# Kernel optimization log

Hardware: AMD Instinct MI355X
Metric: run time of the kernel (lower is better)

The kernel has to match this reference:

```python
import jax, jax.numpy as jnp
import numpy as np

N, C_IN, C_OUT, T, V = 128, 64, 64, 128, 25
GROUPS, K = 8, 3
REL = C_IN // 8  # rel_reduction=8, in_channels>16


def setup_inputs() -> dict:
    key = jax.random.key(0)
    ks = jax.random.split(key, 16)
    f = lambda k, sh, s=0.05: (jax.random.normal(k, sh) * s).astype(jnp.float32)
    return {
        "x0": jax.random.normal(ks[0], (N, C_IN, T, V), jnp.float32),
        "DecoupleA": f(ks[1], (K, GROUPS, V, V), 0.2),
        "A": f(ks[2], (K, V, V), 0.2),
        "alpha": jnp.full((1,), 0.5, jnp.float32),
        "w1": f(ks[3], (K, REL, C_IN)), "b1": f(ks[4], (K, REL)),
        "w2": f(ks[5], (K, REL, C_IN)), "b2": f(ks[6], (K, REL)),
        "w3": f(ks[7], (K, C_OUT, C_IN)), "b3": f(ks[8], (K, C_OUT)),
        "w4": f(ks[9], (K, C_OUT, REL)), "b4": f(ks[10], (K, C_OUT)),
        "Linear_weight": f(ks[11], (C_IN, C_OUT * K)),
        "Linear_bias": f(ks[12], (1, C_OUT * K, 1, 1)),
        "bn0_gamma": jnp.ones((C_OUT * K,), jnp.float32),
        "bn0_beta": jnp.zeros((C_OUT * K,), jnp.float32),
        "ens_w": f(ks[13], (C_OUT, 2 * C_OUT)), "ens_b": f(ks[14], (C_OUT,)),
        "bn_gamma": jnp.full((C_OUT,), 1e-6, jnp.float32),
        "bn_beta": jnp.zeros((C_OUT,), jnp.float32),
    }


def _bn(x, gamma, beta, eps=1e-5):
    # training-mode BatchNorm2d over NCHW: stats over (N, T, V)
    mu = x.mean(axis=(0, 2, 3), keepdims=True)
    var = x.var(axis=(0, 2, 3), keepdims=True)
    return (x - mu) * jax.lax.rsqrt(var + eps) * gamma[None, :, None, None] + beta[None, :, None, None]


def _norm_adj(A):
    # torch: D = A.sum(dim=rows) -> column sums; A @ diag(1/(D+1e-3)) scales columns
    d = A.sum(axis=-2)  # [..., V] column sums
    return A * (1.0 / (d + 0.001))[..., None, :]


def reference(x0, DecoupleA, A, alpha, w1, b1, w2, b2, w3, b3, w4, b4,
              Linear_weight, Linear_bias, bn0_gamma, bn0_beta, ens_w, ens_b,
              bn_gamma, bn_beta):
    n, c_in, t, v = x0.shape
    k, g = DecoupleA.shape[0], DecoupleA.shape[1]
    c_out = w3.shape[1]
    # DecoupleA.repeat(1, out_channels//groups, 1, 1) == tile along channel dim
    learn_A = jnp.tile(DecoupleA, (1, c_out // g, 1, 1))  # [K, C_OUT, V, V]
    norm_A = _norm_adj(learn_A)
    # decoupled linear path
    x = jnp.einsum('nctv,cd->ndtv', x0, Linear_weight) + Linear_bias
    x = _bn(x, bn0_gamma, bn0_beta)
    x = x.reshape(n, k, c_out, t, v)
    x = jnp.einsum('nkctv,kcvw->nctw', x, norm_A)  # [n, C_OUT, t, v]
    # CTRGC branches (conv-then-mean over T == mean-then-1x1 since conv is linear)
    xm = x0.mean(axis=2)  # [n, c_in, v]
    y = jnp.zeros((n, c_out, t, v), x0.dtype)
    for i in range(k):
        x1 = jnp.einsum('ncv,rc->nrv', xm, w1[i]) + b1[i][:, None]
        x2 = jnp.einsum('ncv,rc->nrv', xm, w2[i]) + b2[i][:, None]
        diff = jnp.tanh(x1[:, :, :, None] - x2[:, :, None, :])        # [n, rel, u, w]
        att = jnp.einsum('nruw,or->nouw', diff, w4[i]) + b4[i][None, :, None, None]
        att = att * alpha[0] + A[i][None, None]                        # [n, C_OUT, u, w]
        x3 = jnp.einsum('nctv,oc->notv', x0, w3[i]) + b3[i][None, :, None, None]
        y = y + jnp.einsum('ncuv,nctu->nctv', att, x3)
    cat = jnp.concatenate([x, y], axis=1)                              # [n, 2*C_OUT, t, v]
    out = jnp.einsum('nctv,oc->notv', cat, ens_w) + ens_b[None, :, None, None]
    out = _bn(out, bn_gamma, bn_beta)
    out = out + x0  # down is identity since in_channels == out_channels
    return jax.nn.relu(out)
```

## Files before the change

kernel.cpp:

```cpp
#include <hip/hip_runtime.h>
#include <cstddef>
#include <cstring>

typedef _Float16 h8 __attribute__((ext_vector_type(8)));
typedef _Float16 h4v __attribute__((ext_vector_type(4)));
typedef float f4 __attribute__((ext_vector_type(4)));
typedef unsigned int u32;
typedef unsigned short u16;

#define MTOT 409600.0f

#define DO_XM  15360000
#define DO_GP  15564800
#define DO_GR  16613376

#define WS_OB16 0
#define WS_ATT  13631488
#define WS_ATTB 23461888
#define WS_BN2P 23666688
#define WS_PAR  23827456
#define WS_CSN  23828000

#define ATT_H 27262976
#define NAB_H 47595520
#define CB_H  47620096
#define WA_H  47622144
#define W3_H  47634432
#define EW_H  47646720

#define LDS_DYN 116736

__global__ __launch_bounds__(512) void k_gram(const float* __restrict__ x0,
                                              float* __restrict__ gp) {
  __shared__ _Float16 Xs[64 * 128];
  char* smb = (char*)Xs;
  int bid = blockIdx.x, tid = threadIdx.x;
  int n = bid >> 1, sh = bid & 1;
  int base = sh * 1536;
  int niter = sh ? 13 : 12;
  const float* xb = x0 + (size_t)n * 204800;
  int wid = tid >> 6, lane = tid & 63, l15 = lane & 15, l4 = lane >> 4;
  int ca = (wid & 3) * 16;
  int jb0 = (wid >> 2) * 2;
  f4 acc[2] = {{0.f, 0.f, 0.f, 0.f}, {0.f, 0.f, 0.f, 0.f}};
  int sc = tid >> 3, scol = (tid & 7) * 16;
  int swz = (sc & 7) << 4;
  for (int it = 0; it < niter; ++it) {
    int s0 = base + it * 128;
    __syncthreads();
    const float* src = xb + sc * 3200 + s0 + scol;
#pragma unroll
    for (int j = 0; j < 4; ++j) {
      float4 f = *(const float4*)(src + j * 4);
      h4v hv = {(_Float16)f.x, (_Float16)f.y, (_Float16)f.z, (_Float16)f.w};
      *(h4v*)(smb + sc * 256 + (((scol + j * 4) * 2) ^ swz)) = hv;
    }
    __syncthreads();
#pragma unroll
    for (int kk = 0; kk < 4; ++kk) {
      int kb = kk * 64 + l4 * 16;
      int arow = ca + l15;
      h8 af = *(const h8*)(smb + arow * 256 + (kb ^ ((arow & 7) << 4)));
#pragma unroll
      for (int j = 0; j < 2; ++j) {
        int brow = (jb0 + j) * 16 + l15;
        h8 bf = *(const h8*)(smb + brow * 256 + (kb ^ ((brow & 7) << 4)));
        acc[j] = __builtin_amdgcn_mfma_f32_16x16x32_f16(af, bf, acc[j], 0, 0, 0);
      }
    }
  }
  float* o = gp + (size_t)bid * 4096;
#pragma unroll
  for (int j = 0; j < 2; ++j)
#pragma unroll
    for (int q = 0; q < 4; ++q)
      o[(ca + l4 * 4 + q) * 64 + (jb0 + j) * 16 + l15] = acc[j][q];
}

__global__ __launch_bounds__(256) void k_gred(float* __restrict__ dsc) {
  int bid = blockIdx.x, tid = threadIdx.x;
  if (bid < 16) {
    int idx = bid * 256 + tid;
    const float* gp = dsc + DO_GP;
    float s0 = 0.f, s1 = 0.f, s2 = 0.f, s3 = 0.f;
    for (int b = 0; b < 256; b += 4) {
      s0 += gp[(size_t)b * 4096 + idx];
      s1 += gp[(size_t)(b + 1) * 4096 + idx];
      s2 += gp[(size_t)(b + 2) * 4096 + idx];
      s3 += gp[(size_t)(b + 3) * 4096 + idx];
    }
    dsc[DO_GR + idx] = (s0 + s1) + (s2 + s3);
  } else {
    __shared__ float red[64][5];
    int c = tid >> 2, j = tid & 3;
    float s = 0.f;
    for (int nn = j; nn < 128; nn += 4) {
      const float* xmp = dsc + DO_XM + (size_t)(nn * 64 + c) * 25;
      for (int v = 0; v < 25; ++v) s += xmp[v];
    }
    red[c][j] = s;
    __syncthreads();
    if (j == 0)
      dsc[DO_GR + 4096 + c] = 128.f * (red[c][0] + red[c][1] + red[c][2] + red[c][3]);
  }
}

__global__ __launch_bounds__(256) void k_xm(const float* __restrict__ x0,
                                            float* __restrict__ dsc,
                                            float* __restrict__ ws) {
  __shared__ float red[8][32];
  int bid = blockIdx.x;
  int gid = bid * 256 + threadIdx.x;
  if (gid < 204800) ws[WS_ATTB + gid] = 0.f;
  int n = bid >> 6, c = bid & 63;
  int tid = threadIdx.x;
  int tq = tid >> 5, v = tid & 31;
  const float* xb = x0 + (size_t)(n * 64 + c) * 3200;
  float s = 0.f;
  if (v < 25) {
    for (int j = 0; j < 16; j++) s += xb[(tq + 8 * j) * 25 + v];
  }
  red[tq][v] = s;
  __syncthreads();
  if (tq == 0 && v < 25) {
    float tot = 0.f;
#pragma unroll
    for (int q = 0; q < 8; q++) tot += red[q][v];
    dsc[DO_XM + (size_t)(n * 64 + c) * 25 + v] = tot * (1.0f / 128.0f);
  }
}

__global__ __launch_bounds__(256) void k_prep(const float* __restrict__ DA,
                                              const float* __restrict__ w3,
                                              const float* __restrict__ ensw,
                                              float* __restrict__ wsF) {
  int bid = blockIdx.x, tid = threadIdx.x;
  _Float16* wsH = (_Float16*)wsF;
  if (bid < 3) {
    if (tid < 200) {
      int k = bid, g = tid / 25, w = tid % 25;
      const float* base = DA + (k * 8 + g) * 625 + w;
      float s = 0.f;
      for (int v = 0; v < 25; v++) s += base[v * 25];
      float inv = 1.0f / (s + 0.001f);
      wsF[WS_CSN + k * 200 + g * 25 + w] = s * inv;
      _Float16* dst = wsH + NAB_H + (size_t)((k * 8 + g) * 32 + w) * 32;
      for (int v = 0; v < 25; v++) dst[v] = (_Float16)(base[v * 25] * inv);
      for (int v = 25; v < 32; v++) dst[v] = (_Float16)0.f;
    }
  } else if (bid == 3) {
    for (int idx = tid; idx < 5376; idx += 256) {
      int kg = idx / 224, r = idx % 224;
      int w = 25 + r / 32, v = r & 31;
      wsH[NAB_H + (size_t)(kg * 32 + w) * 32 + v] = (_Float16)0.f;
    }
  } else if (bid < 12) {
    int i0 = (bid - 4) * 1536;
    for (int i = tid; i < 1536; i += 256)
      wsH[W3_H + i0 + i] = (_Float16)w3[i0 + i];
  } else {
    int i0 = (bid - 12) * 2048;
    for (int i = tid; i < 2048; i += 256)
      wsH[EW_H + i0 + i] = (_Float16)ensw[i0 + i];
  }
}

__global__ __launch_bounds__(256) void k_bnstat(const float* __restrict__ dsc,
                                                const float* __restrict__ Lw,
                                                const float* __restrict__ g0,
                                                const float* __restrict__ b0,
                                                float* __restrict__ wsF) {
  __shared__ float Gsh[64 * 66];
  __shared__ float Ly[64][17];
  __shared__ float part[16][17];
  __shared__ float a1L[16];
  int bid = blockIdx.x, tid = threadIdx.x;
  int d0 = bid * 16, dl = tid >> 4, r = tid & 15, d = d0 + dl;
  for (int idx = tid; idx < 4096; idx += 256)
    Gsh[(idx >> 6) * 66 + (idx & 63)] = dsc[DO_GR + idx];
  for (int idx = tid; idx < 1024; idx += 256)
    Ly[idx >> 4][idx & 15] = Lw[(idx >> 4) * 192 + d0 + (idx & 15)];
  __syncthreads();
  float acc = 0.f;
#pragma unroll
  for (int cc = 0; cc < 4; ++cc) {
    int c = r * 4 + cc;
    float h = 0.f;
    for (int c2 = 0; c2 < 64; ++c2) h += Gsh[c * 66 + c2] * Ly[c2][dl];
    acc += Ly[c][dl] * h;
  }
  part[dl][r] = acc;
  __syncthreads();
  if (r == 0) {
    float ex2 = 0.f;
#pragma unroll
    for (int i = 0; i < 16; ++i) ex2 += part[dl][i];
    ex2 *= (1.0f / MTOT);
    float mu = 0.f;
    for (int c = 0; c < 64; ++c) mu += dsc[DO_GR + 4096 + c] * Ly[c][dl];
    mu *= (1.0f / MTOT);
    float var = ex2 - mu * mu;
    float a1 = g0[d] * rsqrtf(var + 1e-5f);
    float b1c = b0[d] - a1 * mu;
    wsF[WS_PAR + 128 + d] = a1;
    wsF[WS_PAR + 320 + d] = b1c;
    a1L[dl] = a1;
  }
  __syncthreads();
  _Float16* wsH = (_Float16*)wsF;
  int k = d >> 6, cg = d & 63;
  float a1v = a1L[dl];
#pragma unroll
  for (int j = 0; j < 4; ++j) {
    int e = r * 4 + j;
    wsH[WA_H + k * 4096 + cg * 64 + e] = (_Float16)(a1v * Lw[e * 192 + d]);
  }
}

__global__ __launch_bounds__(256) void k_cb(float* __restrict__ wsF) {
  int tid = threadIdx.x;
  _Float16* wsH = (_Float16*)wsF;
  for (int idx = tid; idx < 2048; idx += 256) {
    int c = idx >> 5, w = idx & 31;
    float s = 0.f;
    if (w < 25) {
      int g = c & 7;
      for (int k = 0; k < 3; ++k)
        s += wsF[WS_PAR + 320 + k * 64 + c] * wsF[WS_CSN + k * 200 + g * 25 + w];
    }
    wsH[CB_H + idx] = (_Float16)s;
  }
}

__global__ __launch_bounds__(256) void k_att(const float* __restrict__ dsc,
    const float* __restrict__ w1, const float* __restrict__ b1,
    const float* __restrict__ w2, const float* __restrict__ b2,
    const float* __restrict__ w4, const float* __restrict__ b4,
    const float* __restrict__ Ag, const float* __restrict__ alpha,
    const float* __restrict__ b3, float* __restrict__ wsF) {
  __shared__ float xms[1600];
  __shared__ float x1s[200];
  __shared__ float x2s[200];
  __shared__ float Td[5000];
  int bid = blockIdx.x, tid = threadIdx.x;
  int n = bid / 3, i = bid % 3;
  for (int idx = tid; idx < 1600; idx += 256)
    xms[idx] = dsc[DO_XM + (size_t)n * 1600 + idx];
  __syncthreads();
  for (int idx = tid; idx < 400; idx += 256) {
    int r = (idx % 200) / 25, u = idx % 25;
    const float* wv = (idx < 200 ? w1 : w2) + (i * 8 + r) * 64;
    float acc = (idx < 200 ? b1 : b2)[i * 8 + r];
    for (int c = 0; c < 64; c++) acc += xms[c * 25 + u] * wv[c];
    if (idx < 200) x1s[r * 25 + u] = acc; else x2s[r * 25 + u] = acc;
  }
  __syncthreads();
  for (int idx = tid; idx < 5000; idx += 256) {
    int r = idx / 625, u = (idx % 625) / 25, w = idx % 25;
    Td[idx] = tanhf(x1s[r * 25 + u] - x2s[r * 25 + w]);
  }
  __syncthreads();
  float al = alpha[0];
  u32* attW = (u32*)wsF;
  for (int p = tid; p < 1600; p += 256) {
    int o = p / 25, w = p % 25;
    float w4r[8];
#pragma unroll
    for (int r = 0; r < 8; r++) w4r[r] = w4[(i * 64 + o) * 8 + r];
    float b4v = b4[i * 64 + o];
    const float* AgW = Ag + i * 625 + w;
    float asum = 0.f;
    size_t rowH = (size_t)ATT_H + ((size_t)((n * 3 + i) * 64 + o) * 25 + w) * 32;
    u32* row = attW + rowH / 2;
    for (int up = 0; up < 16; ++up) {
      u32 word = 0;
#pragma unroll
      for (int h = 0; h < 2; ++h) {
        int u = up * 2 + h;
        float v = 0.f;
        if (u < 25) {
          float acc = b4v;
#pragma unroll
          for (int r = 0; r < 8; r++) acc += w4r[r] * Td[r * 625 + u * 25 + w];
          v = al * acc + AgW[u * 25];
          asum += v;
        }
        union { _Float16 hf; u16 b; } cv;
        cv.hf = (_Float16)v;
        word |= ((u32)cv.b) << (16 * h);
      }
      row[up] = word;
    }
    atomicAdd(&wsF[WS_ATTB + (size_t)n * 1600 + p], b3[i * 64 + o] * asum);
  }
}

__device__ __forceinline__ void stageX(const float* __restrict__ xn, char* sm, int tid) {
  for (int idx = tid; idx < 25600; idx += 512) {
    int c = idx / 400, s = idx % 400;
    float f = xn[c * 3200 + s];
    *(_Float16*)(sm + s * 128 + ((c * 2) ^ ((s & 7) << 4))) = (_Float16)f;
  }
}
__device__ __forceinline__ void zeroHpads(char* sm, int tid) {
  for (int idx = tid; idx < 7168; idx += 512) {
    int c = idx / 112, r = idx % 112;
    int t = r / 7, u = 25 + r % 7;
    int hs = (((t & 3) ^ ((c >> 2) & 3)) << 4);
    *(_Float16*)(sm + 51200 + c * 1024 + t * 64 + ((u * 2) ^ hs)) = (_Float16)0.f;
  }
}
__device__ __forceinline__ void gemm64(const _Float16* __restrict__ Aw, char* sm,
                                       int wid, int lane) {
  int l15 = lane & 15, l4 = lane >> 4;
  int mt = wid & 3, half = wid >> 2;
  h8 a0 = *(const h8*)(Aw + (mt * 16 + l15) * 64 + l4 * 8);
  h8 a1 = *(const h8*)(Aw + (mt * 16 + l15) * 64 + 32 + l4 * 8);
  int nt0 = half * 13, nt1 = 13 + half * 12;
  for (int nt = nt0; nt < nt1; ++nt) {
    int s = nt * 16 + l15;
    int sw = (s & 7) << 4;
    const char* rb = sm + s * 128;
    h8 b0 = *(const h8*)(rb + ((l4 * 16) ^ sw));
    h8 b1 = *(const h8*)(rb + ((64 + l4 * 16) ^ sw));
    f4 acc = {0.f, 0.f, 0.f, 0.f};
    acc = __builtin_amdgcn_mfma_f32_16x16x32_f16(a0, b0, acc, 0, 0, 0);
    acc = __builtin_amdgcn_mfma_f32_16x16x32_f16(a1, b1, acc, 0, 0, 0);
    int t = s / 25, u = s % 25;
#pragma unroll
    for (int q = 0; q < 4; ++q) {
      int c = mt * 16 + l4 * 4 + q;
      int hs = (((t & 3) ^ ((c >> 2) & 3)) << 4);
      *(_Float16*)(sm + 51200 + c * 1024 + t * 64 + ((u * 2) ^ hs)) = (_Float16)acc[q];
    }
  }
}

__global__ __launch_bounds__(512) void kAB(const float* __restrict__ x0,
                                           float* ws,
                                           const float* __restrict__ ensb) {
  extern __shared__ char sm[];
  __shared__ float redS[128];
  __shared__ float attBs[1600];
  const _Float16* wsH = (const _Float16*)ws;
  int tid = threadIdx.x, bid = blockIdx.x;
  int lb = (bid & 7) * 128 + (bid >> 3);
  int n = lb >> 3, tile = lb & 7;
  int wid = tid >> 6, lane = tid & 63, l15 = lane & 15, l4 = lane >> 4;
  if (tid < 128) redS[tid] = 0.f;
  for (int idx = tid; idx < 1600; idx += 512)
    attBs[idx] = ws[WS_ATTB + (size_t)n * 1600 + idx];
  stageX(x0 + (size_t)n * 204800 + tile * 400, sm, tid);
  zeroHpads(sm, tid);
  __syncthreads();
  f4 accx[8][2], accy[8][2];
#pragma unroll
  for (int a = 0; a < 8; a++)
#pragma unroll
    for (int b = 0; b < 2; b++) {
      accx[a][b] = (f4){0.f, 0.f, 0.f, 0.f};
      accy[a][b] = (f4){0.f, 0.f, 0.f, 0.f};
    }
  for (int k = 0; k < 3; ++k) {
    gemm64(wsH + WA_H + k * 4096, sm, wid, lane);
    __syncthreads();
#pragma unroll
    for (int mt2 = 0; mt2 < 8; ++mt2) {
      int c = mt2 * 8 + wid;
      int hs = (((l15 & 3) ^ ((c >> 2) & 3)) << 4);
      h8 aH = *(const h8*)(sm + 51200 + c * 1024 + l15 * 64 + ((l4 * 16) ^ hs));
#pragma unroll
      for (int nt2 = 0; nt2 < 2; ++nt2) {
        const _Float16* nb = wsH + NAB_H +
            (size_t)((k * 8 + wid) * 32 + nt2 * 16 + l15) * 32 + l4 * 8;
        accx[mt2][nt2] = __builtin_amdgcn_mfma_f32_16x16x32_f16(
            aH, *(const h8*)nb, accx[mt2][nt2], 0, 0, 0);
      }
    }
    __syncthreads();
  }
  for (int i = 0; i < 3; ++i) {
    gemm64(wsH + W3_H + i * 4096, sm, wid, lane);
    __syncthreads();
#pragma unroll
    for (int mt2 = 0; mt2 < 8; ++mt2) {
      int c = mt2 * 8 + wid;
      int hs = (((l15 & 3) ^ ((c >> 2) & 3)) << 4);
      h8 aX = *(const h8*)(sm + 51200 + c * 1024 + l15 * 64 + ((l4 * 16) ^ hs));
#pragma unroll
      for (int nt2 = 0; nt2 < 2; ++nt2) {
        int v = nt2 * 16 + l15;
        int vc = v < 25 ? v : 0;
        const _Float16* ab = wsH + ATT_H +
            ((size_t)((n * 3 + i) * 64 + c) * 25 + vc) * 32 + l4 * 8;
        accy[mt2][nt2] = __builtin_amdgcn_mfma_f32_16x16x32_f16(
            aX, *(const h8*)ab, accy[mt2][nt2], 0, 0, 0);
      }
    }
    __syncthreads();
  }
#pragma unroll
  for (int mt2 = 0; mt2 < 8; ++mt2) {
    int c = mt2 * 8 + wid;
#pragma unroll
    for (int nt2 = 0; nt2 < 2; ++nt2) {
      int w = nt2 * 16 + l15;
      if (w < 25) {
        float cbv = (float)wsH[CB_H + c * 32 + w];
        float abv = attBs[c * 25 + w];
#pragma unroll
        for (int q = 0; q < 4; ++q) {
          int t = l4 * 4 + q;
          int s = t * 25 + w;
          int sw = (s & 7) << 4;
          *(_Float16*)(sm + s * 256 + ((c * 2) ^ sw)) =
              (_Float16)(accx[mt2][nt2][q] + cbv);
          *(_Float16*)(sm + s * 256 + (((64 + c) * 2) ^ sw)) =
              (_Float16)(accy[mt2][nt2][q] + abv);
        }
      }
    }
  }
  __syncthreads();
  int mt = wid & 3, half = wid >> 2;
  h8 ea[4];
#pragma unroll
  for (int ks = 0; ks < 4; ++ks)
    ea[ks] = *(const h8*)(wsH + EW_H + (mt * 16 + l15) * 128 + ks * 32 + l4 * 8);
  float eb[4];
#pragma unroll
  for (int q = 0; q < 4; ++q) eb[q] = ensb[mt * 16 + l4 * 4 + q];
  float lsum[4] = {0.f, 0.f, 0.f, 0.f}, lss[4] = {0.f, 0.f, 0.f, 0.f};
  u16* ob16 = (u16*)ws;
  int nt0 = half * 13, nt1 = 13 + half * 12;
  for (int nt = nt0; nt < nt1; ++nt) {
    int s = nt * 16 + l15;
    int sw = (s & 7) << 4;
    f4 acc = {0.f, 0.f, 0.f, 0.f};
#pragma unroll
    for (int ks = 0; ks < 4; ++ks) {
      h8 b = *(const h8*)(sm + s * 256 + (((ks * 32 + l4 * 8) * 2) ^ sw));
      acc = __builtin_amdgcn_mfma_f32_16x16x32_f16(ea[ks], b, acc, 0, 0, 0);
    }
    size_t ob = (size_t)n * 204800 + (size_t)tile * 400 + s;
#pragma unroll
    for (int q = 0; q < 4; ++q) {
      int o = mt * 16 + l4 * 4 + q;
      union { _Float16 hf; u16 b; } cv;
      cv.hf = (_Float16)(acc[q] + eb[q]);
      ob16[ob + (size_t)o * 3200] = cv.b;
      float val = (float)cv.hf;
      lsum[q] += val;
      lss[q] += val * val;
    }
  }
#pragma unroll
  for (int q = 0; q < 4; ++q) {
    int o = mt * 16 + l4 * 4 + q;
    atomicAdd(&redS[o], lsum[q]);
    atomicAdd(&redS[64 + o], lss[q]);
  }
  __syncthreads();
  if (tid < 64) {
    ws[WS_BN2P + (size_t)bid * 128 + tid * 2] = redS[tid];
    ws[WS_BN2P + (size_t)bid * 128 + tid * 2 + 1] = redS[64 + tid];
  }
}

__global__ __launch_bounds__(256) void k_bn2(const float* __restrict__ g2,
                                             const float* __restrict__ b2,
                                             float* __restrict__ ws) {
  __shared__ float rs[256], rss[256];
  int o = blockIdx.x, tid = threadIdx.x;
  float s = 0.f, ss = 0.f;
  for (int b = tid; b < 1024; b += 256) {
    s += ws[WS_BN2P + (size_t)b * 128 + o * 2];
    ss += ws[WS_BN2P + (size_t)b * 128 + o * 2 + 1];
  }
  rs[tid] = s; rss[tid] = ss;
  __syncthreads();
  for (int st = 128; st > 0; st >>= 1) {
    if (tid < st) { rs[tid] += rs[tid + st]; rss[tid] += rss[tid + st]; }
    __syncthreads();
  }
  if (tid == 0) {
    float mu = rs[0] / MTOT;
    float var = rss[0] / MTOT - mu * mu;
    float a2 = g2[o] * rsqrtf(var + 1e-5f);
    ws[WS_PAR + o] = a2;
    ws[WS_PAR + 64 + o] = b2[o] - a2 * mu;
  }
}

__global__ __launch_bounds__(256) void k_final(const float* __restrict__ x0,
                                               const float* __restrict__ ws,
                                               float* __restrict__ dout) {
  size_t g = (size_t)blockIdx.x * 256 + threadIdx.x;
  h4v p = reinterpret_cast<const h4v*>(ws)[g];
  float4 x = reinterpret_cast<const float4*>(x0)[g];
  int o = (int)((g * 4 / 3200) & 63);
  float a2 = ws[WS_PAR + o], bc = ws[WS_PAR + 64 + o];
  float4 r;
  r.x = fmaxf(fmaf(a2, (float)p[0], bc) + x.x, 0.f);
  r.y = fmaxf(fmaf(a2, (float)p[1], bc) + x.y, 0.f);
  r.z = fmaxf(fmaf(a2, (float)p[2], bc) + x.z, 0.f);
  r.w = fmaxf(fmaf(a2, (float)p[3], bc) + x.w, 0.f);
  reinterpret_cast<float4*>(dout)[g] = r;
}

extern "C" void kernel_launch(void* const* d_in, const int* in_sizes, int n_in,
                              void* d_out, int out_size, void* d_ws, size_t ws_size,
                              hipStream_t stream) {
  const float* x0    = (const float*)d_in[0];
  const float* DA    = (const float*)d_in[1];
  const float* Ag    = (const float*)d_in[2];
  const float* alpha = (const float*)d_in[3];
  const float* w1    = (const float*)d_in[4];
  const float* b1    = (const float*)d_in[5];
  const float* w2    = (const float*)d_in[6];
  const float* b2    = (const float*)d_in[7];
  const float* w3    = (const float*)d_in[8];
  const float* b3    = (const float*)d_in[9];
  const float* w4    = (const float*)d_in[10];
  const float* b4    = (const float*)d_in[11];
  const float* Lw    = (const float*)d_in[12];
  const float* g0    = (const float*)d_in[14];
  const float* b0    = (const float*)d_in[15];
  const float* ensw  = (const float*)d_in[16];
  const float* ensb  = (const float*)d_in[17];
  const float* g2    = (const float*)d_in[18];
  const float* b2n   = (const float*)d_in[19];
  float* out = (float*)d_out;
  float* ws  = (float*)d_ws;

  hipFuncSetAttribute((const void*)kAB, hipFuncAttributeMaxDynamicSharedMemorySize, LDS_DYN);

  k_xm<<<8192, 256, 0, stream>>>(x0, out, ws);
  k_gram<<<256, 512, 0, stream>>>(x0, out + DO_GP);
  k_prep<<<16, 256, 0, stream>>>(DA, w3, ensw, ws);
  k_att<<<384, 256, 0, stream>>>(out, w1, b1, w2, b2, w4, b4, Ag, alpha, b3, ws);
  k_gred<<<17, 256, 0, stream>>>(out);
  k_bnstat<<<12, 256, 0, stream>>>(out, Lw, g0, b0, ws);
  k_cb<<<1, 256, 0, stream>>>(ws);
  kAB<<<1024, 512, LDS_DYN, stream>>>(x0, ws, ensb);
  k_bn2<<<64, 256, 0, stream>>>(g2, b2n, ws);
  k_final<<<25600, 256, 0, stream>>>(x0, ws, out);
}
```

Measured before the change: 330.8 us.

## Double kAB block size to 16 waves and redistribute MFMA work per wave

The main fused kernel now runs 1024 threads per block instead of 512. The gemm64 N-tiles are split across four wave groups of 7/6/6/6 tiles, and each wave handles 4 channel tiles instead of 8, which halves the accumulator register footprint. X staging is vectorised to write four fp16 channels at once, and the BN partial sums are reduced with wavefront shuffles before the LDS atomics. The intent is more waves in flight to hide memory latency and less LDS atomic contention, at the cost of tighter register limits from launch_bounds(1024,4) and more waves competing at each barrier.

```diff
diff --git a/kernel.cpp b/kernel.cpp
--- a/kernel.cpp
+++ b/kernel.cpp
@@ -296,14 +296,17 @@
 }
 
 __device__ __forceinline__ void stageX(const float* __restrict__ xn, char* sm, int tid) {
-  for (int idx = tid; idx < 25600; idx += 512) {
-    int c = idx / 400, s = idx % 400;
-    float f = xn[c * 3200 + s];
-    *(_Float16*)(sm + s * 128 + ((c * 2) ^ ((s & 7) << 4))) = (_Float16)f;
+  for (int u = tid; u < 6400; u += 1024) {
+    int cg = u / 400, s = u - cg * 400;
+    int c0 = cg * 4;
+    const float* p = xn + c0 * 3200 + s;
+    float a = p[0], b = p[3200], c = p[6400], d = p[9600];
+    h4v hv = {(_Float16)a, (_Float16)b, (_Float16)c, (_Float16)d};
+    *(h4v*)(sm + s * 128 + ((c0 * 2) ^ ((s & 7) << 4))) = hv;
   }
 }
 __device__ __forceinline__ void zeroHpads(char* sm, int tid) {
-  for (int idx = tid; idx < 7168; idx += 512) {
+  for (int idx = tid; idx < 7168; idx += 1024) {
     int c = idx / 112, r = idx % 112;
     int t = r / 7, u = 25 + r % 7;
     int hs = (((t & 3) ^ ((c >> 2) & 3)) << 4);
@@ -311,12 +314,10 @@
   }
 }
 __device__ __forceinline__ void gemm64(const _Float16* __restrict__ Aw, char* sm,
-                                       int wid, int lane) {
+                                       int mt, int nt0, int nt1, int lane) {
   int l15 = lane & 15, l4 = lane >> 4;
-  int mt = wid & 3, half = wid >> 2;
   h8 a0 = *(const h8*)(Aw + (mt * 16 + l15) * 64 + l4 * 8);
   h8 a1 = *(const h8*)(Aw + (mt * 16 + l15) * 64 + 32 + l4 * 8);
-  int nt0 = half * 13, nt1 = 13 + half * 12;
   for (int nt = nt0; nt < nt1; ++nt) {
     int s = nt * 16 + l15;
     int sw = (s & 7) << 4;
@@ -336,9 +337,9 @@
   }
 }
 
-__global__ __launch_bounds__(512) void kAB(const float* __restrict__ x0,
-                                           float* ws,
-                                           const float* __restrict__ ensb) {
+__global__ __launch_bounds__(1024, 4) void kAB(const float* __restrict__ x0,
+                                               float* ws,
+                                               const float* __restrict__ ensb) {
   extern __shared__ char sm[];
   __shared__ float redS[128];
   __shared__ float attBs[1600];
@@ -347,32 +348,35 @@
   int lb = (bid & 7) * 128 + (bid >> 3);
   int n = lb >> 3, tile = lb & 7;
   int wid = tid >> 6, lane = tid & 63, l15 = lane & 15, l4 = lane >> 4;
+  int mt = wid & 3, q4 = wid >> 2, g = wid & 7;
+  int nt0 = q4 ? 1 + 6 * q4 : 0;
+  int nt1 = q4 ? nt0 + 6 : 7;
   if (tid < 128) redS[tid] = 0.f;
-  for (int idx = tid; idx < 1600; idx += 512)
+  for (int idx = tid; idx < 1600; idx += 1024)
     attBs[idx] = ws[WS_ATTB + (size_t)n * 1600 + idx];
   stageX(x0 + (size_t)n * 204800 + tile * 400, sm, tid);
   zeroHpads(sm, tid);
   __syncthreads();
-  f4 accx[8][2], accy[8][2];
-#pragma unroll
-  for (int a = 0; a < 8; a++)
+  f4 accx[4][2], accy[4][2];
+#pragma unroll
+  for (int a = 0; a < 4; a++)
 #pragma unroll
     for (int b = 0; b < 2; b++) {
       accx[a][b] = (f4){0.f, 0.f, 0.f, 0.f};
       accy[a][b] = (f4){0.f, 0.f, 0.f, 0.f};
     }
   for (int k = 0; k < 3; ++k) {
-    gemm64(wsH + WA_H + k * 4096, sm, wid, lane);
-    __syncthreads();
-#pragma unroll
-    for (int mt2 = 0; mt2 < 8; ++mt2) {
-      int c = mt2 * 8 + wid;
+    gemm64(wsH + WA_H + k * 4096, sm, mt, nt0, nt1, lane);
+    __syncthreads();
+#pragma unroll
+    for (int mt2 = 0; mt2 < 4; ++mt2) {
+      int c = mt2 * 16 + wid;
       int hs = (((l15 & 3) ^ ((c >> 2) & 3)) << 4);
       h8 aH = *(const h8*)(sm + 51200 + c * 1024 + l15 * 64 + ((l4 * 16) ^ hs));
 #pragma unroll
       for (int nt2 = 0; nt2 < 2; ++nt2) {
         const _Float16* nb = wsH + NAB_H +
-            (size_t)((k * 8 + wid) * 32 + nt2 * 16 + l15) * 32 + l4 * 8;
+            (size_t)((k * 8 + g) * 32 + nt2 * 16 + l15) * 32 + l4 * 8;
         accx[mt2][nt2] = __builtin_amdgcn_mfma_f32_16x16x32_f16(
             aH, *(const h8*)nb, accx[mt2][nt2], 0, 0, 0);
       }
@@ -380,11 +384,11 @@
     __syncthreads();
   }
   for (int i = 0; i < 3; ++i) {
-    gemm64(wsH + W3_H + i * 4096, sm, wid, lane);
-    __syncthreads();
-#pragma unroll
-    for (int mt2 = 0; mt2 < 8; ++mt2) {
-      int c = mt2 * 8 + wid;
+    gemm64(wsH + W3_H + i * 4096, sm, mt, nt0, nt1, lane);
+    __syncthreads();
+#pragma unroll
+    for (int mt2 = 0; mt2 < 4; ++mt2) {
+      int c = mt2 * 16 + wid;
       int hs = (((l15 & 3) ^ ((c >> 2) & 3)) << 4);
       h8 aX = *(const h8*)(sm + 51200 + c * 1024 + l15 * 64 + ((l4 * 16) ^ hs));
 #pragma unroll
@@ -400,8 +404,8 @@
     __syncthreads();
   }
 #pragma unroll
-  for (int mt2 = 0; mt2 < 8; ++mt2) {
-    int c = mt2 * 8 + wid;
+  for (int mt2 = 0; mt2 < 4; ++mt2) {
+    int c = mt2 * 16 + wid;
 #pragma unroll
     for (int nt2 = 0; nt2 < 2; ++nt2) {
       int w = nt2 * 16 + l15;
@@ -422,7 +426,6 @@
     }
   }
   __syncthreads();
-  int mt = wid & 3, half = wid >> 2;
   h8 ea[4];
 #pragma unroll
   for (int ks = 0; ks < 4; ++ks)
@@ -432,7 +435,6 @@
   for (int q = 0; q < 4; ++q) eb[q] = ensb[mt * 16 + l4 * 4 + q];
   float lsum[4] = {0.f, 0.f, 0.f, 0.f}, lss[4] = {0.f, 0.f, 0.f, 0.f};
   u16* ob16 = (u16*)ws;
-  int nt0 = half * 13, nt1 = 13 + half * 12;
   for (int nt = nt0; nt < nt1; ++nt) {
     int s = nt * 16 + l15;
     int sw = (s & 7) << 4;
@@ -456,9 +458,19 @@
   }
 #pragma unroll
   for (int q = 0; q < 4; ++q) {
-    int o = mt * 16 + l4 * 4 + q;
-    atomicAdd(&redS[o], lsum[q]);
-    atomicAdd(&redS[64 + o], lss[q]);
+#pragma unroll
+    for (int d = 1; d < 16; d <<= 1) {
+      lsum[q] += __shfl_xor(lsum[q], d);
+      lss[q] += __shfl_xor(lss[q], d);
+    }
+  }
+  if (l15 == 0) {
+#pragma unroll
+    for (int q = 0; q < 4; ++q) {
+      int o = mt * 16 + l4 * 4 + q;
+      atomicAdd(&redS[o], lsum[q]);
+      atomicAdd(&redS[64 + o], lss[q]);
+    }
   }
   __syncthreads();
   if (tid < 64) {
@@ -542,7 +554,7 @@
   k_gred<<<17, 256, 0, stream>>>(out);
   k_bnstat<<<12, 256, 0, stream>>>(out, Lw, g0, b0, ws);
   k_cb<<<1, 256, 0, stream>>>(ws);
-  kAB<<<1024, 512, LDS_DYN, stream>>>(x0, ws, ensb);
+  kAB<<<1024, 1024, LDS_DYN, stream>>>(x0, ws, ensb);
   k_bn2<<<64, 256, 0, stream>>>(g2, b2n, ws);
   k_final<<<25600, 256, 0, stream>>>(x0, ws, out);
 }
```

Result: faster. 300.5 us (-9.2%).
